# Kernel optimization log

Hardware: AMD Instinct MI355X
Metric: run time of the kernel (lower is better)

## Reference

```python
import jax, jax.numpy as jnp
import numpy as np

B, C, H, W = 32, 512, 32, 32


def setup_inputs() -> dict:
    key = jax.random.key(0)
    ks = jax.random.split(key, 7)
    c2 = C // 2
    s_in = (1.0 / C) ** 0.5   # torch Conv2d default init scale (kernel 1x1)
    s_c2 = (1.0 / c2) ** 0.5
    return {
        "x": jax.random.normal(ks[0], (B, C, H, W), jnp.float32),
        "Wk": jax.random.normal(ks[1], (c2, C), jnp.float32) * s_in,
        "bk": jax.random.normal(ks[2], (c2,), jnp.float32) * s_in,
        "Wv": jax.random.normal(ks[3], (c2, C), jnp.float32) * s_in,
        "bv": jax.random.normal(ks[4], (c2,), jnp.float32) * s_in,
        "Wo": jax.random.normal(ks[5], (C, c2), jnp.float32) * s_c2,
        "bo": jax.random.normal(ks[6], (C,), jnp.float32) * s_c2,
    }


def reference(x, Wk, bk, Wv, bv, Wo, bo):
    Bn, Cn, Hn, Wn = x.shape
    c2 = Cn // 2
    M = Hn * Wn
    # 1x1 convs as channel contractions
    k = jnp.einsum('oc,bchw->bohw', Wk, x) + bk[None, :, None, None]   # [B,c2,H,W]
    v = jnp.einsum('oc,bchw->bohw', Wv, x) + bv[None, :, None, None]   # [B,c2,H,W]
    # torch .reshape(B, M, c2) reinterprets memory (NOT a transpose) -> same in jnp
    v = v.reshape(Bn, M, c2)                                           # [B,M,c2]
    kf = k.reshape(Bn, c2, M)                                          # [B,c2,M]
    # cov_feature: k^T I_hat k with I_hat = (1/M)I - (1/M^2)11^T
    #            = (1/M) k^T k - (1/M^2) s s^T,  s = sum over channels
    gram = jnp.einsum('bcm,bcn->bmn', kf, kf) / M                      # [B,M,M]
    s = kf.sum(axis=1)                                                 # [B,M]
    cov = gram - (s[:, :, None] * s[:, None, :]) / (M * M)
    attn = jax.nn.softmax(cov * (c2 ** -0.5), axis=-1)                 # [B,M,M]
    out = jnp.einsum('bmn,bnc->bmc', attn, v)                          # [B,M,c2]
    # torch .view(B, c2, H, W) is also a raw memory reinterpretation
    out = out.reshape(Bn, c2, Hn, Wn)
    out = jnp.einsum('oc,bchw->bohw', Wo, out) + bo[None, :, None, None]
    return out + x
```

## Files before the change

### kernel.cpp

```cpp
#include <hip/hip_runtime.h>


typedef short bf8 __attribute__((ext_vector_type(8)));
typedef float f32x4 __attribute__((ext_vector_type(4)));

#define MFMA16(a, b, c) __builtin_amdgcn_mfma_f32_16x16x32_bf16((a), (b), (c), 0, 0, 0)

__device__ __forceinline__ short f2bf(float x) {
  unsigned u = __float_as_uint(x);
  u += 0x7fffu + ((u >> 16) & 1u);
  return (short)(u >> 16);
}

__device__ __forceinline__ void gll16(const short* g, void* l) {
  __builtin_amdgcn_global_load_lds(
      (const __attribute__((address_space(1))) unsigned int*)g,
      (__attribute__((address_space(3))) unsigned int*)l, 16, 0, 0);
}

__device__ __forceinline__ void lgkm0() {
  asm volatile("s_waitcnt lgkmcnt(0)" ::: "memory");
}
template <int N>
__device__ __forceinline__ void waitv() {
  static_assert(N == 0 || N == 4 || N == 8, "bad vmcnt");
  if constexpr (N == 0) asm volatile("s_waitcnt vmcnt(0)" ::: "memory");
  else if constexpr (N == 4) asm volatile("s_waitcnt vmcnt(4)" ::: "memory");
  else asm volatile("s_waitcnt vmcnt(8)" ::: "memory");
}
__device__ __forceinline__ void barrier_relaxed() {
  asm volatile("" ::: "memory");
  __builtin_amdgcn_s_barrier();
  asm volatile("" ::: "memory");
}

__device__ __forceinline__ void gemm_core(const short* __restrict__ A,
                                          const short* __restrict__ B,
                                          int ldA, int ldB, int ksteps,
                                          char* smem, f32x4 acc[4][4]) {
  const int tid = threadIdx.x;
  const int w = tid >> 6, l = tid & 63;
  const int q = l >> 4, i = l & 15;
  const int wm = w & 1, wn = w >> 1;
  const int srow = l >> 3;
  const int gcol = ((l & 7) ^ srow) * 8;
  f32x4 zz = {0.f, 0.f, 0.f, 0.f};
  #pragma unroll
  for (int mt = 0; mt < 4; ++mt)
    #pragma unroll
    for (int nt = 0; nt < 4; ++nt) acc[mt][nt] = zz;

  for (int ks = 0; ks < ksteps; ++ks) {
    __syncthreads();
    const short* Ak = A + ks * 64 + gcol;
    const short* Bk = B + ks * 64 + gcol;
    #pragma unroll
    for (int j = 0; j < 4; ++j) {
      int s = w * 4 + j;
      size_t row = (size_t)(s * 8 + srow);
      gll16(Ak + row * ldA, smem + s * 1024);
      gll16(Bk + row * ldB, smem + 16384 + s * 1024);
    }
    __syncthreads();
    #pragma unroll
    for (int kq = 0; kq < 2; ++kq) {
      int sw = ((kq * 4 + q) ^ (i & 7)) * 16;
      bf8 af[4], bq[4];
      #pragma unroll
      for (int mt = 0; mt < 4; ++mt)
        af[mt] = *(const bf8*)(smem + (wm * 64 + mt * 16 + i) * 128 + sw);
      #pragma unroll
      for (int nt = 0; nt < 4; ++nt)
        bq[nt] = *(const bf8*)(smem + 16384 + (wn * 64 + nt * 16 + i) * 128 + sw);
      #pragma unroll
      for (int mt = 0; mt < 4; ++mt)
        #pragma unroll
        for (int nt = 0; nt < 4; ++nt)
          acc[mt][nt] = MFMA16(af[mt], bq[nt], acc[mt][nt]);
    }
  }
}

__global__ __launch_bounds__(256) void p0_fused(const float* __restrict__ x,
                                                short* __restrict__ xT,
                                                const float* __restrict__ Wk,
                                                const float* __restrict__ Wv,
                                                const float* __restrict__ Wo,
                                                short* __restrict__ Wkv_bf,
                                                short* __restrict__ Wo_bf) {
  __shared__ float lds[64][65];
  int id = blockIdx.x;
  int t = threadIdx.x;
  if (id >= 4096) {
    int g = (id - 4096) * 256 + t;
    if (g < 262144) {
      int o = g >> 9, c = g & 511;
      float v = (o < 256) ? Wk[o * 512 + c] : Wv[(o - 256) * 512 + c];
      Wkv_bf[g] = f2bf(v);
    } else {
      int i2 = g - 262144;
      Wo_bf[i2] = f2bf(Wo[i2]);
    }
    return;
  }
  int cb = id & 7, sb = (id >> 3) & 15, b = id >> 7;
  int c0 = cb * 64, sp0 = sb * 64;
  const float4* x4 = reinterpret_cast<const float4*>(x);
  #pragma unroll
  for (int j = 0; j < 4; ++j) {
    int lin = t + 256 * j;
    int cl = lin >> 4, s4 = lin & 15;
    float4 v = x4[(((size_t)b * 512 + c0 + cl) * 1024 + sp0 + s4 * 4) >> 2];
    lds[cl][s4 * 4 + 0] = v.x; lds[cl][s4 * 4 + 1] = v.y;
    lds[cl][s4 * 4 + 2] = v.z; lds[cl][s4 * 4 + 3] = v.w;
  }
  __syncthreads();
  int spl = t >> 2, cs = (t & 3) * 16;
  bf8 o0, o1;
  #pragma unroll
  for (int j = 0; j < 8; ++j) o0[j] = f2bf(lds[cs + j][spl]);
  #pragma unroll
  for (int j = 0; j < 8; ++j) o1[j] = f2bf(lds[cs + 8 + j][spl]);
  size_t base = ((size_t)b * 1024 + sp0 + spl) * 512 + c0 + cs;
  *reinterpret_cast<bf8*>(xT + base) = o0;
  *reinterpret_cast<bf8*>(xT + base + 8) = o1;
}

__global__ __launch_bounds__(256, 2) void k1_kv(const short* __restrict__ xT,
                                                const short* __restrict__ Wkv,
                                                const float* __restrict__ bk,
                                                const float* __restrict__ bv,
                                                short* __restrict__ kT,
                                                short* __restrict__ vT,
                                                float* __restrict__ s_part) {
  __shared__ __attribute__((aligned(16))) char smem[36864];
  f32x4 acc[4][4];
  int id = blockIdx.x;
  int xcd = id & 7, slot = id >> 3;
  int bm = xcd * 32 + (slot >> 2);
  int bn = slot & 3;
  gemm_core(xT + (size_t)bm * 128 * 512, Wkv + (size_t)bn * 128 * 512,
            512, 512, 8, smem, acc);
  int tid = threadIdx.x;
  int w = tid >> 6, l = tid & 63, q = l >> 4, i = l & 15;
  int wm = w & 1, wn = w >> 1;
  int mbase = bm * 128 + wm * 64;
  int nbase = bn * 128 + wn * 64;
  if (bn < 2) {
    __syncthreads();
    short* st = (short*)smem + w * 4352;
    float rp[4][4];
    #pragma unroll
    for (int mt = 0; mt < 4; ++mt)
      #pragma unroll
      for (int r = 0; r < 4; ++r) rp[mt][r] = 0.f;
    #pragma unroll
    for (int mt = 0; mt < 4; ++mt)
      #pragma unroll
      for (int nt = 0; nt < 4; ++nt) {
        float bias = bk[nbase + nt * 16 + i];
        #pragma unroll
        for (int r = 0; r < 4; ++r) {
          float val = acc[mt][nt][r] + bias;
          st[(mt * 16 + q * 4 + r) * 68 + nt * 16 + i] = f2bf(val);
          rp[mt][r] += val;
        }
      }
    lgkm0();
    #pragma unroll
    for (int j = 0; j < 8; ++j) {
      int row = j * 8 + (l >> 3), cc = l & 7;
      bf8 vv = *(const bf8*)(st + row * 68 + cc * 8);
      *(bf8*)(kT + (size_t)(mbase + row) * 256 + nbase + cc * 8) = vv;
    }
    #pragma unroll
    for (int mask = 1; mask <= 8; mask <<= 1)
      #pragma unroll
      for (int mt = 0; mt < 4; ++mt)
        #pragma unroll
        for (int r = 0; r < 4; ++r) rp[mt][r] += __shfl_xor(rp[mt][r], mask, 64);
    if (i == 0) {
      int pg = bn * 2 + wn;
      #pragma unroll
      for (int mt = 0; mt < 4; ++mt)
        #pragma unroll
        for (int r = 0; r < 4; ++r)
          s_part[pg * 32768 + mbase + mt * 16 + q * 4 + r] = rp[mt][r];
    }
  } else {
    #pragma unroll
    for (int mt = 0; mt < 4; ++mt)
      #pragma unroll
      for (int nt = 0; nt < 4; ++nt) {
        int o2 = nbase + nt * 16 + i - 256;
        float bias = bv[o2];
        #pragma unroll
        for (int r = 0; r < 4; ++r) {
          float val = acc[mt][nt][r] + bias;
          int mg = mbase + mt * 16 + q * 4 + r;
          int b = mg >> 10, sp = mg & 1023;
          vT[((size_t)b * 256 + (sp & 255)) * 1024 + 4 * o2 + (sp >> 8)] = f2bf(val);
        }
      }
  }
}

__global__ __launch_bounds__(256, 2) void k2_fused(const short* __restrict__ kT,
                                                   const short* __restrict__ vT,
                                                   const float* __restrict__ s_part,
                                                   short* __restrict__ OB) {
  __shared__ __attribute__((aligned(16))) char smem[81920];
  char* Apan = smem;
  char* Ppan = smem + 32768;
  char* Bst  = smem + 49152;

  const int id = blockIdx.x;
  const int xcd = id & 7, slot = id >> 3;
  const int b  = xcd * 4 + (slot >> 4);
  const int bm = slot & 15;

  const int tid = threadIdx.x;
  const int w = tid >> 6, l = tid & 63;
  const int q = l >> 4, i = l & 15;
  const int srow = l >> 3;
  const int gcol = ((l & 7) ^ srow) * 8;

  const short* kTb = kT + (size_t)b * 1024 * 256;
  const short* vTb = vT + (size_t)b * 256 * 1024;

  char* slabA = Bst + w * 4096;
  char* slabB = Bst + 16384 + w * 4096;

  const float sc1 = 1.0f / 16384.0f;
  const float sc2 = 1.0f / 16777216.0f;

  {
    const short* Am = kTb + (size_t)bm * 64 * 256;
    #pragma unroll
    for (int ks = 0; ks < 4; ++ks)
      #pragma unroll
      for (int j2 = 0; j2 < 2; ++j2) {
        int s2 = w * 2 + j2;
        gll16(Am + (size_t)(s2 * 8 + srow) * 256 + ks * 64 + gcol,
              Apan + ks * 8192 + s2 * 1024);
      }
  }

  const int mglob = b * 1024;
  float sm2[4][4];
  #pragma unroll
  for (int mt = 0; mt < 4; ++mt)
    #pragma unroll
    for (int r = 0; r < 4; ++r) {
      int m = mglob + bm * 64 + mt * 16 + q * 4 + r;
      sm2[mt][r] = (s_part[m] + s_part[32768 + m] + s_part[65536 + m] +
                    s_part[98304 + m]) * sc2;
    }
  float sn[8][2];
  #pragma unroll
  for (int c = 0; c < 8; ++c)
    #pragma unroll
    for (int nt = 0; nt < 2; ++nt) {
      int m = mglob + c * 128 + w * 32 + nt * 16 + i;
      sn[c][nt] = s_part[m] + s_part[32768 + m] + s_part[65536 + m] +
                  s_part[98304 + m];
    }

  auto stageS = [&](int c, int ks, char* sl) {
    const short* Bn = kTb + (size_t)c * 128 * 256 + ks * 64 + gcol;
    #pragma unroll
    for (int j = 0; j < 4; ++j)
      gll16(Bn + (size_t)(w * 32 + j * 8 + srow) * 256, sl + j * 1024);
  };
  auto stageV = [&](int c, int ks2, int h, char* sl) {
    const short* Vn = vTb + c * 128 + ks2 * 64 + gcol;
    #pragma unroll
    for (int j = 0; j < 4; ++j)
      gll16(Vn + (size_t)(w * 64 + h * 32 + j * 8 + srow) * 1024, sl + j * 1024);
  };

  stageS(0, 0, slabA);
  stageS(0, 1, slabB);
  waitv<8>();
  barrier_relaxed();

  f32x4 zz = {0.f, 0.f, 0.f, 0.f};
  f32x4 acc_o[4][4];
  float rowsum[4][4];
  #pragma unroll
  for (int mt = 0; mt < 4; ++mt)
    #pragma unroll
    for (int ct = 0; ct < 4; ++ct) acc_o[mt][ct] = zz;
  #pragma unroll
  for (int mt = 0; mt < 4; ++mt)
    #pragma unroll
    for (int r = 0; r < 4; ++r) rowsum[mt][r] = 0.f;

  #pragma unroll
  for (int c = 0; c < 8; ++c) {
    f32x4 acc_s[4][2];
    #pragma unroll
    for (int mt = 0; mt < 4; ++mt)
      #pragma unroll
      for (int nt = 0; nt < 2; ++nt) acc_s[mt][nt] = zz;

    #pragma unroll
    for (int ks = 0; ks < 4; ++ks) {
      char* sl = (ks & 1) ? slabB : slabA;
      waitv<4>();
      #pragma unroll
      for (int kq = 0; kq < 2; ++kq) {
        int sw = ((kq * 4 + q) ^ (i & 7)) * 16;
        bf8 af[4], bq2[2];
        #pragma unroll
        for (int mt = 0; mt < 4; ++mt)
          af[mt] = *(const bf8*)(Apan + ks * 8192 + (mt * 16 + i) * 128 + sw);
        #pragma unroll
        for (int nt = 0; nt < 2; ++nt)
          bq2[nt] = *(const bf8*)(sl + (nt * 16 + i) * 128 + sw);
        __builtin_amdgcn_s_setprio(1);
        #pragma unroll
        for (int mt = 0; mt < 4; ++mt)
          #pragma unroll
          for (int nt = 0; nt < 2; ++nt)
            acc_s[mt][nt] = MFMA16(af[mt], bq2[nt], acc_s[mt][nt]);
        __builtin_amdgcn_s_setprio(0);
      }
      lgkm0();
      if (ks < 2) stageS(c, ks + 2, sl);
      else        stageV(c, 0, ks - 2, sl);
    }

    barrier_relaxed();
    #pragma unroll
    for (int nt = 0; nt < 2; ++nt) {
      float snv = sn[c][nt];
      int nl = w * 32 + nt * 16 + i;
      char* pbase = Ppan + (nl >> 6) * 8192 + (nl & 7) * 2;
      int gchunk = (nl >> 3) & 7;
      #pragma unroll
      for (int mt = 0; mt < 4; ++mt)
        #pragma unroll
        for (int r = 0; r < 4; ++r) {
          int ml = mt * 16 + q * 4 + r;
          float p = __expf(acc_s[mt][nt][r] * sc1 - sm2[mt][r] * snv);
          rowsum[mt][r] += p;
          *(short*)(pbase + ml * 128 + ((gchunk ^ (ml & 7)) * 16)) = f2bf(p);
        }
    }
    lgkm0();
    barrier_relaxed();

    #pragma unroll
    for (int pv = 0; pv < 4; ++pv) {
      char* sl = (pv & 1) ? slabB : slabA;
      const int ks2 = pv >> 1, h = pv & 1;
      if (c == 7 && pv == 3) waitv<0>(); else waitv<4>();
      #pragma unroll
      for (int kq = 0; kq < 2; ++kq) {
        int sw = ((kq * 4 + q) ^ (i & 7)) * 16;
        bf8 ap[4], bv2[2];
        #pragma unroll
        for (int mt = 0; mt < 4; ++mt)
          ap[mt] = *(const bf8*)(Ppan + ks2 * 8192 + (mt * 16 + i) * 128 + sw);
        #pragma unroll
        for (int u = 0; u < 2; ++u)
          bv2[u] = *(const bf8*)(sl + (u * 16 + i) * 128 + sw);
        __builtin_amdgcn_s_setprio(1);
        #pragma unroll
        for (int mt = 0; mt < 4; ++mt)
          #pragma unroll
          for (int u = 0; u < 2; ++u)
            acc_o[mt][h * 2 + u] = MFMA16(ap[mt], bv2[u], acc_o[mt][h * 2 + u]);
        __builtin_amdgcn_s_setprio(0);
      }
      lgkm0();
      if (pv < 2) stageV(c, 1, pv, sl);
      else if (c < 7) stageS(c + 1, pv - 2, sl);
    }
  }

  #pragma unroll
  for (int mask = 1; mask <= 8; mask <<= 1)
    #pragma unroll
    for (int mt = 0; mt < 4; ++mt)
      #pragma unroll
      for (int r = 0; r < 4; ++r) rowsum[mt][r] += __shfl_xor(rowsum[mt][r], mask, 64);
  __syncthreads();
  float* rs = (float*)Ppan;
  if (i == 0) {
    #pragma unroll
    for (int mt = 0; mt < 4; ++mt)
      #pragma unroll
      for (int r = 0; r < 4; ++r)
        rs[w * 64 + mt * 16 + q * 4 + r] = rowsum[mt][r];
  }
  __syncthreads();
  float rinv[4][4];
  #pragma unroll
  for (int mt = 0; mt < 4; ++mt)
    #pragma unroll
    for (int r = 0; r < 4; ++r) {
      int m = mt * 16 + q * 4 + r;
      rinv[mt][r] = 1.0f / (rs[m] + rs[64 + m] + rs[128 + m] + rs[192 + m]);
    }
  short* ob = (short*)(Bst + w * 8192);
  #pragma unroll
  for (int mt = 0; mt < 4; ++mt)
    #pragma unroll
    for (int ct = 0; ct < 4; ++ct)
      #pragma unroll
      for (int r = 0; r < 4; ++r)
        ob[(r * 64 + ct * 16 + i) * 16 + mt * 4 + q] =
            f2bf(acc_o[mt][ct][r] * rinv[mt][r]);
  short* obg = OB + (size_t)b * 1024 * 256;
  #pragma unroll
  for (int jj = 0; jj < 8; ++jj) {
    int lr = jj * 32 + (l >> 1), ch = l & 1;
    bf8 vv = *(const bf8*)(ob + lr * 16 + ch * 8);
    int rr = lr >> 6, cc = lr & 63;
    *(bf8*)(obg + ((size_t)(rr * 256 + w * 64 + cc)) * 256 + bm * 16 + ch * 8) = vv;
  }
}

__global__ __launch_bounds__(256, 2) void k3_out(const short* __restrict__ Wo_bf,
                                                 const short* __restrict__ OB,
                                                 const float* __restrict__ bo,
                                                 const float* __restrict__ x,
                                                 float* __restrict__ out) {
  __shared__ __attribute__((aligned(16))) char smem[36864];
  f32x4 acc[4][4];
  int id = blockIdx.x;
  int xcd = id & 7, slot = id >> 3;
  int b = xcd * 4 + (slot >> 5);
  int rem = slot & 31;
  int bn = rem >> 2, bm = rem & 3;
  gemm_core(Wo_bf + (size_t)bm * 128 * 256,
            OB + ((size_t)b * 1024 + bn * 128) * 256, 256, 256, 4, smem, acc);
  int tid = threadIdx.x;
  int w = tid >> 6, l = tid & 63, q = l >> 4, i = l & 15;
  int wm = w & 1, wn = w >> 1;
  int oloc = bm * 128 + wm * 64, sploc = bn * 128 + wn * 64;
  __syncthreads();
  float* st = (float*)smem + w * 2112;
  #pragma unroll
  for (int half = 0; half < 2; ++half) {
    if (half) lgkm0();
    #pragma unroll
    for (int mtl = 0; mtl < 2; ++mtl) {
      int mt = half * 2 + mtl;
      #pragma unroll
      for (int nt = 0; nt < 4; ++nt)
        #pragma unroll
        for (int r = 0; r < 4; ++r)
          st[(mtl * 16 + q * 4 + r) * 66 + nt * 16 + i] = acc[mt][nt][r];
    }
    lgkm0();
    #pragma unroll
    for (int j = 0; j < 8; ++j) {
      int row = j * 4 + (l >> 4), c4 = l & 15;
      f32x4 v = *(const f32x4*)(st + row * 66 + c4 * 4);
      int o = oloc + half * 32 + row;
      int sp = sploc + c4 * 4;
      size_t idx = ((size_t)b * 512 + o) * 1024 + sp;
      float4 xv = *(const float4*)(x + idx);
      float bias = bo[o];
      float4 ov;
      ov.x = v[0] + bias + xv.x;
      ov.y = v[1] + bias + xv.y;
      ov.z = v[2] + bias + xv.z;
      ov.w = v[3] + bias + xv.w;
      *(float4*)(out + idx) = ov;
    }
  }
}

extern "C" void kernel_launch(void* const* d_in, const int* in_sizes, int n_in,
                              void* d_out, int out_size, void* d_ws, size_t ws_size,
                              hipStream_t stream) {
  (void)in_sizes; (void)n_in; (void)out_size; (void)ws_size;
  const float* x  = (const float*)d_in[0];
  const float* Wk = (const float*)d_in[1];
  const float* bk = (const float*)d_in[2];
  const float* Wv = (const float*)d_in[3];
  const float* bv = (const float*)d_in[4];
  const float* Wo = (const float*)d_in[5];
  const float* bo = (const float*)d_in[6];
  float* out = (float*)d_out;
  char* ws = (char*)d_ws;

  short* xT     = (short*)(ws);
  short* OB     = (short*)(ws);
  short* kTb    = (short*)(ws + 33554432);
  short* vTb    = (short*)(ws + 50331648);
  short* Wkv_bf = (short*)(ws + 67108864);
  short* Wo_bf  = (short*)(ws + 67633152);
  float* s_part = (float*)(ws + 67895296);

  p0_fused<<<5632, 256, 0, stream>>>(x, xT, Wk, Wv, Wo, Wkv_bf, Wo_bf);
  k1_kv<<<1024, 256, 0, stream>>>(xT, Wkv_bf, bk, bv, kTb, vTb, s_part);
  k2_fused<<<512, 256, 0, stream>>>(kTb, vTb, s_part, OB);
  k3_out<<<1024, 256, 0, stream>>>(Wo_bf, OB, bo, x, out);
}
```

Baseline: 222.5 us.

## Remap V-projection tiles so scattered vT writes become coalesced row stores via LDS

The V half of the k1 projection GEMM now gathers its A-tile rows in a permuted order: four groups of 32 spatial positions, spaced 256 apart, taken from one batch. The reshaped vT rows for a tile then become contiguous. Results are staged in LDS and written out as 16-byte vector stores, replacing scattered 2-byte stores with a stride of 1024 elements. This adds an LDS round trip and a templated load-address variant, and changes the block-to-tile mapping for the V blocks.

```diff
diff --git a/kernel.cpp b/kernel.cpp
--- a/kernel.cpp
+++ b/kernel.cpp
@@ -34,6 +34,7 @@
   asm volatile("" ::: "memory");
 }
 
+template <bool VPERM>
 __device__ __forceinline__ void gemm_core(const short* __restrict__ A,
                                           const short* __restrict__ B,
                                           int ldA, int ldB, int ksteps,
@@ -57,9 +58,10 @@
     #pragma unroll
     for (int j = 0; j < 4; ++j) {
       int s = w * 4 + j;
-      size_t row = (size_t)(s * 8 + srow);
-      gll16(Ak + row * ldA, smem + s * 1024);
-      gll16(Bk + row * ldB, smem + 16384 + s * 1024);
+      size_t arow = VPERM ? (size_t)(w * 256 + j * 8 + srow)
+                          : (size_t)(s * 8 + srow);
+      gll16(Ak + arow * ldA, smem + s * 1024);
+      gll16(Bk + (size_t)(s * 8 + srow) * ldB, smem + 16384 + s * 1024);
     }
     __syncthreads();
     #pragma unroll
@@ -137,16 +139,17 @@
   f32x4 acc[4][4];
   int id = blockIdx.x;
   int xcd = id & 7, slot = id >> 3;
-  int bm = xcd * 32 + (slot >> 2);
-  int bn = slot & 3;
-  gemm_core(xT + (size_t)bm * 128 * 512, Wkv + (size_t)bn * 128 * 512,
-            512, 512, 8, smem, acc);
   int tid = threadIdx.x;
   int w = tid >> 6, l = tid & 63, q = l >> 4, i = l & 15;
   int wm = w & 1, wn = w >> 1;
-  int mbase = bm * 128 + wm * 64;
-  int nbase = bn * 128 + wn * 64;
-  if (bn < 2) {
+
+  if (slot < 64) {
+    int bm = xcd * 32 + (slot >> 1);
+    int bn = slot & 1;
+    gemm_core<false>(xT + (size_t)bm * 128 * 512, Wkv + (size_t)bn * 128 * 512,
+                     512, 512, 8, smem, acc);
+    int mbase = bm * 128 + wm * 64;
+    int nbase = bn * 128 + wn * 64;
     __syncthreads();
     short* st = (short*)smem + w * 4352;
     float rp[4][4];
@@ -188,20 +191,38 @@
           s_part[pg * 32768 + mbase + mt * 16 + q * 4 + r] = rp[mt][r];
     }
   } else {
-    #pragma unroll
-    for (int mt = 0; mt < 4; ++mt)
+    int u = slot - 64;
+    int b = xcd * 4 + (u >> 4);
+    int rem = u & 15;
+    int s0 = (rem >> 1) * 32;
+    int bn = 2 + (rem & 1);
+    gemm_core<true>(xT + ((size_t)b * 1024 + s0) * 512,
+                    Wkv + (size_t)bn * 128 * 512, 512, 512, 8, smem, acc);
+    __syncthreads();
+    short* st = (short*)smem;
+    #pragma unroll
+    for (int mt = 0; mt < 4; ++mt) {
+      int hi2 = wm * 2 + (mt >> 1);
+      int r16 = (mt & 1) * 16;
       #pragma unroll
       for (int nt = 0; nt < 4; ++nt) {
-        int o2 = nbase + nt * 16 + i - 256;
+        int o2 = (bn - 2) * 128 + wn * 64 + nt * 16 + i;
         float bias = bv[o2];
-        #pragma unroll
-        for (int r = 0; r < 4; ++r) {
-          float val = acc[mt][nt][r] + bias;
-          int mg = mbase + mt * 16 + q * 4 + r;
-          int b = mg >> 10, sp = mg & 1023;
-          vT[((size_t)b * 256 + (sp & 255)) * 1024 + 4 * o2 + (sp >> 8)] = f2bf(val);
-        }
+        int col = 4 * (wn * 64 + nt * 16 + i) + hi2;
+        #pragma unroll
+        for (int r = 0; r < 4; ++r)
+          st[(r16 + q * 4 + r) * 520 + col] = f2bf(acc[mt][nt][r] + bias);
       }
+    }
+    __syncthreads();
+    short* vrow = vT + ((size_t)(b * 256 + s0)) * 1024 + (size_t)(bn - 2) * 512;
+    #pragma unroll
+    for (int ii = 0; ii < 8; ++ii) {
+      int kp = tid + 256 * ii;
+      int row = kp >> 6, cc = kp & 63;
+      bf8 vv = *(const bf8*)(st + row * 520 + cc * 8);
+      *(bf8*)(vrow + (size_t)row * 1024 + cc * 8) = vv;
+    }
   }
 }
 
@@ -435,8 +456,9 @@
   int b = xcd * 4 + (slot >> 5);
   int rem = slot & 31;
   int bn = rem >> 2, bm = rem & 3;
-  gemm_core(Wo_bf + (size_t)bm * 128 * 256,
-            OB + ((size_t)b * 1024 + bn * 128) * 256, 256, 256, 4, smem, acc);
+  gemm_core<false>(Wo_bf + (size_t)bm * 128 * 256,
+                   OB + ((size_t)b * 1024 + bn * 128) * 256, 256, 256, 4,
+                   smem, acc);
   int tid = threadIdx.x;
   int w = tid >> 6, l = tid & 63, q = l >> 4, i = l & 15;
   int wm = w & 1, wn = w >> 1;
```

Result: no change. 221.7 us (-0.4%).
